# Kernel optimization log

Hardware: AMD Instinct MI355X
Metric: run time of the kernel (lower is better)

## Reference

```python
import jax, jax.numpy as jnp
import numpy as np

N = 50000      # nodes
E = 800000     # edges (before self loops)
F_IN = 256     # input features
C = 64         # out_channels per head
H = 4          # heads
NC = 3         # num_class


def setup_inputs() -> dict:
    key = jax.random.key(0)
    ks = jax.random.split(key, 11)
    s = 0.1
    return {
        "x": jax.random.normal(ks[0], (N, F_IN), jnp.float32),
        "edge_index": jax.random.randint(ks[1], (2, E), 0, N, dtype=jnp.int64),
        # conv1: in=F_IN -> H*C, concat
        "W1": jax.random.normal(ks[2], (H * C, F_IN), jnp.float32) * s,
        "as1": jax.random.normal(ks[3], (H, C), jnp.float32) * s,
        "ad1": jax.random.normal(ks[4], (H, C), jnp.float32) * s,
        "b1": jnp.zeros((H * C,), jnp.float32),
        # conv2: in=H*C -> H*C, concat
        "W2": jax.random.normal(ks[5], (H * C, H * C), jnp.float32) * s,
        "as2": jax.random.normal(ks[6], (H, C), jnp.float32) * s,
        "ad2": jax.random.normal(ks[7], (H, C), jnp.float32) * s,
        "b2": jnp.zeros((H * C,), jnp.float32),
        # conv3: in=H*C -> NC, heads averaged (concat=False)
        "W3": jax.random.normal(ks[8], (H * NC, H * C), jnp.float32) * s,
        "as3": jax.random.normal(ks[9], (H, NC), jnp.float32) * s,
        "ad3": jax.random.normal(ks[10], (H, NC), jnp.float32) * s,
        "b3": jnp.zeros((NC,), jnp.float32),
    }


def _gat_conv(x, src, dst, W, a_src, a_dst, b, concat):
    # x: [N,F]; src/dst: [E'] (self loops included); W: [H*C, F]; a_*: [H,C]
    n = x.shape[0]
    h_, c_ = a_src.shape
    h = (x @ W.T).reshape(n, h_, c_)                       # [N,H,C]
    alpha_src = (h * a_src[None]).sum(-1)                  # [N,H]
    alpha_dst = (h * a_dst[None]).sum(-1)                  # [N,H]
    e = jax.nn.leaky_relu(alpha_src[src] + alpha_dst[dst], 0.2)  # [E',H]
    # segment softmax over destination-node neighborhoods
    m = jax.ops.segment_max(e, dst, num_segments=n)        # [N,H]
    ex = jnp.exp(e - m[dst])
    den = jax.ops.segment_sum(ex, dst, num_segments=n)     # [N,H]
    alpha = ex / den[dst]                                  # [E',H]
    out = jax.ops.segment_sum(h[src] * alpha[:, :, None], dst, num_segments=n)  # [N,H,C]
    if concat:
        return out.reshape(n, h_ * c_) + b
    return out.mean(axis=1) + b


def reference(x, edge_index, W1, as1, ad1, b1, W2, as2, ad2, b2, W3, as3, ad3, b3):
    n = x.shape[0]
    loop = jnp.arange(n, dtype=edge_index.dtype)
    src = jnp.concatenate([edge_index[0], loop])  # add_self_loops=True
    dst = jnp.concatenate([edge_index[1], loop])
    x = jax.nn.elu(_gat_conv(x, src, dst, W1, as1, ad1, b1, True))
    x = jax.nn.elu(_gat_conv(x, src, dst, W2, as2, ad2, b2, True))
    x = jax.nn.elu(_gat_conv(x, src, dst, W3, as3, ad3, b3, False))
    return x
```

## Files before the change

kernel.cpp:

```cpp
#include <hip/hip_runtime.h>
#include <hip/hip_fp16.h>
#include <cstdint>
#include <cstddef>

#define NNODES 50000
#define NEDGES 800000
#define E2 (NEDGES + NNODES)
#define HC 256

typedef __attribute__((ext_vector_type(8))) short short8v;
typedef __attribute__((ext_vector_type(4))) float f32x4;
typedef const __attribute__((address_space(1))) void* gas_t;
typedef __attribute__((address_space(3))) void* las_t;


__global__ void zero_int(int* __restrict__ p, int n) {
    int i = blockIdx.x * 256 + threadIdx.x;
    if (i < n) p[i] = 0;
}

__global__ void count_deg(const int* __restrict__ ei, int* __restrict__ deg) {
    int i = blockIdx.x * 256 + threadIdx.x;
    if (i >= E2) return;
    int d = (i < NEDGES) ? ei[NEDGES + i] : (i - NEDGES);
    atomicAdd(&deg[d], 1);
}

__global__ void scan1(const int* __restrict__ deg, int* __restrict__ rp, int* __restrict__ bs) {
    __shared__ int s[256];
    int t = threadIdx.x, i = blockIdx.x * 256 + t;
    int v = (i < NNODES) ? deg[i] : 0;
    s[t] = v;
    __syncthreads();
    for (int o = 1; o < 256; o <<= 1) {
        int add = (t >= o) ? s[t - o] : 0;
        __syncthreads();
        s[t] += add;
        __syncthreads();
    }
    if (i < NNODES) rp[i] = s[t] - v;
    if (t == 255) bs[blockIdx.x] = s[255];
}

__global__ void scan2(int* __restrict__ bs, int nb) {
    __shared__ int s[256];
    int t = threadIdx.x;
    int v = (t < nb) ? bs[t] : 0;
    s[t] = v;
    __syncthreads();
    for (int o = 1; o < 256; o <<= 1) {
        int add = (t >= o) ? s[t - o] : 0;
        __syncthreads();
        s[t] += add;
        __syncthreads();
    }
    bs[t] = s[t] - v;
}

__global__ void scan3(int* __restrict__ rp, const int* __restrict__ bs, int* __restrict__ cnt) {
    int i = blockIdx.x * 256 + threadIdx.x;
    if (i < NNODES) {
        int v = rp[i] + bs[blockIdx.x];
        rp[i] = v;
        cnt[i] = v;
    }
    if (i == 0) rp[NNODES] = E2;
}

__global__ void fill_csr(const int* __restrict__ ei, int* __restrict__ cnt, int* __restrict__ csr) {
    int i = blockIdx.x * 256 + threadIdx.x;
    if (i >= E2) return;
    int s, d;
    if (i < NEDGES) { s = ei[i]; d = ei[NEDGES + i]; }
    else            { s = d = i - NEDGES; }
    int pos = atomicAdd(&cnt[d], 1);
    csr[pos] = s;
}


__device__ __forceinline__ unsigned short f2bf(float f) {
    uint32_t u = __float_as_uint(f);
    uint32_t r = (u + 0x7FFFu + ((u >> 16) & 1u)) >> 16;
    return (unsigned short)r;
}
__device__ __forceinline__ float bf2f(unsigned short h) {
    return __uint_as_float(((uint32_t)h) << 16);
}

__global__ void split_bf16(const float* __restrict__ in, unsigned short* __restrict__ hi,
                           unsigned short* __restrict__ lo, int n4) {
    int i = blockIdx.x * 256 + threadIdx.x;
    if (i >= n4) return;
    float4 v = ((const float4*)in)[i];
    unsigned short h0 = f2bf(v.x), h1 = f2bf(v.y), h2 = f2bf(v.z), h3 = f2bf(v.w);
    unsigned short l0 = f2bf(v.x - bf2f(h0));
    unsigned short l1 = f2bf(v.y - bf2f(h1));
    unsigned short l2 = f2bf(v.z - bf2f(h2));
    unsigned short l3 = f2bf(v.w - bf2f(h3));
    uint2 hp, lp;
    hp.x = (uint32_t)h0 | ((uint32_t)h1 << 16);
    hp.y = (uint32_t)h2 | ((uint32_t)h3 << 16);
    lp.x = (uint32_t)l0 | ((uint32_t)l1 << 16);
    lp.y = (uint32_t)l2 | ((uint32_t)l3 << 16);
    *(uint2*)(hi + 4 * (size_t)i) = hp;
    *(uint2*)(lo + 4 * (size_t)i) = lp;
}


__global__ __launch_bounds__(256, 2) void gemm_mfma(
    const unsigned short* __restrict__ Ah, const unsigned short* __restrict__ Al,
    const unsigned short* __restrict__ Wh, const unsigned short* __restrict__ Wl,
    _Float16* __restrict__ out16, int M) {
    __shared__ unsigned short sAh[2][128][32], sAl[2][128][32], sWh[2][128][32], sWl[2][128][32];
    const int t = threadIdx.x;
    const int m0 = blockIdx.x * 128, n0 = blockIdx.y * 128;
    const int lane = t & 63, w = t >> 6;
    const int wr = w >> 1, wc = w & 1;
    const int fr = lane & 15, fg = lane >> 4;

    const int u0 = (w * 2) * 64 + lane, u1 = (w * 2 + 1) * 64 + lane;
    const int row0 = u0 >> 2, cb0 = (u0 & 3) * 8;
    const int row1 = u1 >> 2, cb1 = (u1 & 3) * 8;
    int gra0 = m0 + row0; gra0 = gra0 < M ? gra0 : M - 1;
    int gra1 = m0 + row1; gra1 = gra1 < M ? gra1 : M - 1;
    const int grw0 = n0 + row0, grw1 = n0 + row1;

    auto stage = [&](int b, int kc) {
        __builtin_amdgcn_global_load_lds((gas_t)(Ah + (size_t)gra0 * HC + kc + cb0), (las_t)&sAh[b][row0][cb0], 16, 0, 0);
        __builtin_amdgcn_global_load_lds((gas_t)(Ah + (size_t)gra1 * HC + kc + cb1), (las_t)&sAh[b][row1][cb1], 16, 0, 0);
        __builtin_amdgcn_global_load_lds((gas_t)(Al + (size_t)gra0 * HC + kc + cb0), (las_t)&sAl[b][row0][cb0], 16, 0, 0);
        __builtin_amdgcn_global_load_lds((gas_t)(Al + (size_t)gra1 * HC + kc + cb1), (las_t)&sAl[b][row1][cb1], 16, 0, 0);
        __builtin_amdgcn_global_load_lds((gas_t)(Wh + (size_t)grw0 * HC + kc + cb0), (las_t)&sWh[b][row0][cb0], 16, 0, 0);
        __builtin_amdgcn_global_load_lds((gas_t)(Wh + (size_t)grw1 * HC + kc + cb1), (las_t)&sWh[b][row1][cb1], 16, 0, 0);
        __builtin_amdgcn_global_load_lds((gas_t)(Wl + (size_t)grw0 * HC + kc + cb0), (las_t)&sWl[b][row0][cb0], 16, 0, 0);
        __builtin_amdgcn_global_load_lds((gas_t)(Wl + (size_t)grw1 * HC + kc + cb1), (las_t)&sWl[b][row1][cb1], 16, 0, 0);
    };

    f32x4 acc[4][4];
#pragma unroll
    for (int mi = 0; mi < 4; mi++)
#pragma unroll
        for (int ni = 0; ni < 4; ni++) acc[mi][ni] = (f32x4){0.f, 0.f, 0.f, 0.f};

    auto compute = [&](int b) {
        short8v ah[4], al[4], bh[4], bl[4];
#pragma unroll
        for (int i = 0; i < 4; i++) {
            ah[i] = *(const short8v*)&sAh[b][wr * 64 + i * 16 + fr][fg * 8];
            al[i] = *(const short8v*)&sAl[b][wr * 64 + i * 16 + fr][fg * 8];
            bh[i] = *(const short8v*)&sWh[b][wc * 64 + i * 16 + fr][fg * 8];
            bl[i] = *(const short8v*)&sWl[b][wc * 64 + i * 16 + fr][fg * 8];
        }
#pragma unroll
        for (int mi = 0; mi < 4; mi++)
#pragma unroll
            for (int ni = 0; ni < 4; ni++) {
                acc[mi][ni] = __builtin_amdgcn_mfma_f32_16x16x32_bf16(ah[mi], bh[ni], acc[mi][ni], 0, 0, 0);
                acc[mi][ni] = __builtin_amdgcn_mfma_f32_16x16x32_bf16(ah[mi], bl[ni], acc[mi][ni], 0, 0, 0);
                acc[mi][ni] = __builtin_amdgcn_mfma_f32_16x16x32_bf16(al[mi], bh[ni], acc[mi][ni], 0, 0, 0);
            }
    };

    stage(0, 0);
    __syncthreads();
#pragma unroll
    for (int kt = 0; kt < 7; kt++) {
        stage((kt + 1) & 1, (kt + 1) * 32);
        compute(kt & 1);
        __syncthreads();
    }
    compute(1);

#pragma unroll
    for (int mi = 0; mi < 4; mi++) {
#pragma unroll
        for (int r = 0; r < 4; r++) {
            int gr = m0 + wr * 64 + mi * 16 + fg * 4 + r;
            if (gr < M) {
#pragma unroll
                for (int ni = 0; ni < 4; ni++) {
                    out16[(size_t)gr * HC + n0 + wc * 64 + ni * 16 + fr] = (_Float16)acc[mi][ni][r];
                }
            }
        }
    }
}


__global__ void alpha_hc(const _Float16* __restrict__ h16, const float* __restrict__ a_s,
                         const float* __restrict__ a_d, float* __restrict__ asrc,
                         float* __restrict__ adst) {
    int n = blockIdx.x * 4 + (threadIdx.x >> 6);
    int lane = threadIdx.x & 63;
    uint2 raw = *(const uint2*)(h16 + (size_t)n * HC + lane * 4);
    __half2 p0 = *(__half2*)&raw.x;
    __half2 p1 = *(__half2*)&raw.y;
    float h0 = __low2float(p0), h1 = __high2float(p0);
    float h2 = __low2float(p1), h3 = __high2float(p1);
    float4 s4 = *(const float4*)(a_s + lane * 4);
    float4 d4 = *(const float4*)(a_d + lane * 4);
    float ps = h0 * s4.x + h1 * s4.y + h2 * s4.z + h3 * s4.w;
    float pd = h0 * d4.x + h1 * d4.y + h2 * d4.z + h3 * d4.w;
#pragma unroll
    for (int o = 1; o < 16; o <<= 1) {
        ps += __shfl_xor(ps, o);
        pd += __shfl_xor(pd, o);
    }
    if ((lane & 15) == 0) {
        int hh = lane >> 4;
        asrc[n * 4 + hh] = ps;
        adst[n * 4 + hh] = pd;
    }
}


#define CHUNK 512

__global__ void aggregate_hc(const _Float16* __restrict__ h16, const float* __restrict__ asrc,
                             const float* __restrict__ adst, const int* __restrict__ rp,
                             const int* __restrict__ csr, const float* __restrict__ bias,
                             float* __restrict__ y, unsigned short* __restrict__ yh,
                             unsigned short* __restrict__ yl, int flags) {
    __shared__ int   sIdx[CHUNK];
    __shared__ float sE4[CHUNK][4];
    __shared__ float sM[4][4], sS[4][4];
    __shared__ float sRed[4][32][9];
    int n = blockIdx.x;
    int t = threadIdx.x;
    int r0 = rp[n], deg = rp[n + 1] - r0;

    if (deg <= CHUNK) {
        for (int j = t; j < deg; j += 256) sIdx[j] = csr[r0 + j];
        __syncthreads();

        int hA = t & 3, jj = t >> 2;
        float adh = adst[n * 4 + hA];
        float pm = -1e30f;
        for (int j = jj; j < deg; j += 64) {
            int s = sIdx[j];
            float e = asrc[s * 4 + hA] + adh;
            e = e > 0.f ? e : 0.2f * e;
            sE4[j][hA] = e;
            pm = fmaxf(pm, e);
        }
#pragma unroll
        for (int o = 4; o <= 32; o <<= 1) pm = fmaxf(pm, __shfl_xor(pm, o));
        if ((t & 63) < 4) sM[t >> 6][t & 3] = pm;
        __syncthreads();

        float mh = fmaxf(fmaxf(sM[0][hA], sM[1][hA]), fmaxf(sM[2][hA], sM[3][hA]));
        float ps = 0.f;
        for (int j = jj; j < deg; j += 64) {
            float ex = __expf(sE4[j][hA] - mh);
            sE4[j][hA] = ex;
            ps += ex;
        }
#pragma unroll
        for (int o = 4; o <= 32; o <<= 1) ps += __shfl_xor(ps, o);
        if ((t & 63) < 4) sS[t >> 6][t & 3] = ps;
        __syncthreads();

        int G = t >> 5, q = t & 31, hh = q >> 3;
        float a[8];
#pragma unroll
        for (int i = 0; i < 8; i++) a[i] = 0.f;
#pragma unroll 2
        for (int j = G; j < deg; j += 8) {
            int s = sIdx[j];
            float aw = sE4[j][hh];
            uint4 raw = *(const uint4*)(h16 + (size_t)s * HC + 8 * q);
            const _Float16* hv = reinterpret_cast<const _Float16*>(&raw);
#pragma unroll
            for (int i = 0; i < 8; i++) a[i] = fmaf((float)hv[i], aw, a[i]);
        }
#pragma unroll
        for (int i = 0; i < 8; i++) a[i] += __shfl_xor(a[i], 32);
        int wv = t >> 6, l = t & 63;
        if (l < 32) {
#pragma unroll
            for (int i = 0; i < 8; i++) sRed[wv][l][i] = a[i];
        }
        __syncthreads();

        int c = t;
        float val = sRed[0][c >> 3][c & 7] + sRed[1][c >> 3][c & 7]
                  + sRed[2][c >> 3][c & 7] + sRed[3][c >> 3][c & 7];
        int ch = c >> 6;
        float ssum = sS[0][ch] + sS[1][ch] + sS[2][ch] + sS[3][ch];
        float outv = val / ssum + bias[c];
        outv = outv > 0.f ? outv : expm1f(outv);
        size_t off = (size_t)n * HC + c;
        if (flags & 1) y[off] = outv;
        if (flags & 2) {
            unsigned short hi = f2bf(outv);
            yh[off] = hi;
            yl[off] = f2bf(outv - bf2f(hi));
        }
    } else {
        int w = t >> 6, l = t & 63;
        float ad = adst[n * 4 + w];
        int hoff = (w << 6) + l;
        const _Float16* hp = h16 + hoff;
        float m = -1e30f;
        for (int j = l; j < deg; j += 64) {
            int s = csr[r0 + j];
            float e = asrc[s * 4 + w] + ad;
            e = e > 0.f ? e : 0.2f * e;
            m = fmaxf(m, e);
        }
#pragma unroll
        for (int o = 32; o > 0; o >>= 1) m = fmaxf(m, __shfl_xor(m, o));
        float acc = 0.f, ssum = 0.f;
        for (int j = 0; j < deg; j++) {
            int s = csr[r0 + j];
            float e = asrc[s * 4 + w] + ad;
            e = e > 0.f ? e : 0.2f * e;
            float aa = __expf(e - m);
            ssum += aa;
            acc = fmaf(aa, (float)hp[(size_t)s * HC], acc);
        }
        float outv = acc / ssum + bias[hoff];
        outv = outv > 0.f ? outv : expm1f(outv);
        size_t off = (size_t)n * HC + hoff;
        if (flags & 1) y[off] = outv;
        if (flags & 2) {
            unsigned short hi = f2bf(outv);
            yh[off] = hi;
            yl[off] = f2bf(outv - bf2f(hi));
        }
    }
}


__global__ void gemm_small(const float* __restrict__ Y, const float* __restrict__ W3,
                           float* __restrict__ h3) {
    int idx = blockIdx.x * 256 + threadIdx.x;
    if (idx >= NNODES * 12) return;
    int n = idx / 12, o = idx - n * 12;
    const float4* xr = (const float4*)(Y + (size_t)n * HC);
    const float4* wr = (const float4*)(W3 + o * HC);
    float acc = 0.f;
#pragma unroll 8
    for (int k = 0; k < 64; k++) {
        float4 a = xr[k], b = wr[k];
        acc += a.x * b.x + a.y * b.y + a.z * b.z + a.w * b.w;
    }
    h3[idx] = acc;
}

__global__ void alpha3(const float* __restrict__ h3, const float* __restrict__ a_s,
                       const float* __restrict__ a_d, float* __restrict__ asrc,
                       float* __restrict__ adst) {
    int n = blockIdx.x * 256 + threadIdx.x;
    if (n >= NNODES) return;
    const float* hr = h3 + (size_t)n * 12;
    float s[4], d[4];
#pragma unroll
    for (int hh = 0; hh < 4; hh++) {
        s[hh] = hr[hh * 3] * a_s[hh * 3] + hr[hh * 3 + 1] * a_s[hh * 3 + 1] + hr[hh * 3 + 2] * a_s[hh * 3 + 2];
        d[hh] = hr[hh * 3] * a_d[hh * 3] + hr[hh * 3 + 1] * a_d[hh * 3 + 1] + hr[hh * 3 + 2] * a_d[hh * 3 + 2];
    }
    *(float4*)(asrc + n * 4) = make_float4(s[0], s[1], s[2], s[3]);
    *(float4*)(adst + n * 4) = make_float4(d[0], d[1], d[2], d[3]);
}

__global__ void aggregate3(const float* __restrict__ h3, const float* __restrict__ asrc,
                           const float* __restrict__ adst, const int* __restrict__ rp,
                           const int* __restrict__ csr, const float* __restrict__ b3,
                           float* __restrict__ out) {
    int n = blockIdx.x * 4 + (threadIdx.x >> 6);
    int l = threadIdx.x & 63;
    if (n >= NNODES) return;
    int r0 = rp[n], deg = rp[n + 1] - r0;
    float4 ad = *(const float4*)(adst + n * 4);

    float m0 = -1e30f, m1 = -1e30f, m2 = -1e30f, m3 = -1e30f;
    for (int j = l; j < deg; j += 64) {
        int s = csr[r0 + j];
        float4 a4 = *(const float4*)(asrc + s * 4);
        float e0 = a4.x + ad.x, e1 = a4.y + ad.y, e2 = a4.z + ad.z, e3 = a4.w + ad.w;
        e0 = e0 > 0.f ? e0 : 0.2f * e0;
        e1 = e1 > 0.f ? e1 : 0.2f * e1;
        e2 = e2 > 0.f ? e2 : 0.2f * e2;
        e3 = e3 > 0.f ? e3 : 0.2f * e3;
        m0 = fmaxf(m0, e0); m1 = fmaxf(m1, e1); m2 = fmaxf(m2, e2); m3 = fmaxf(m3, e3);
    }
    for (int o = 32; o > 0; o >>= 1) {
        m0 = fmaxf(m0, __shfl_xor(m0, o));
        m1 = fmaxf(m1, __shfl_xor(m1, o));
        m2 = fmaxf(m2, __shfl_xor(m2, o));
        m3 = fmaxf(m3, __shfl_xor(m3, o));
    }

    float acc[12];
#pragma unroll
    for (int k = 0; k < 12; k++) acc[k] = 0.f;
    float s0 = 0.f, s1 = 0.f, s2 = 0.f, s3 = 0.f;
    for (int j = l; j < deg; j += 64) {
        int s = csr[r0 + j];
        float4 a4 = *(const float4*)(asrc + s * 4);
        float e0 = a4.x + ad.x, e1 = a4.y + ad.y, e2 = a4.z + ad.z, e3 = a4.w + ad.w;
        e0 = e0 > 0.f ? e0 : 0.2f * e0;
        e1 = e1 > 0.f ? e1 : 0.2f * e1;
        e2 = e2 > 0.f ? e2 : 0.2f * e2;
        e3 = e3 > 0.f ? e3 : 0.2f * e3;
        float w0 = __expf(e0 - m0), w1 = __expf(e1 - m1), w2 = __expf(e2 - m2), w3 = __expf(e3 - m3);
        s0 += w0; s1 += w1; s2 += w2; s3 += w3;
        const float* hr = h3 + (size_t)s * 12;
#pragma unroll
        for (int c = 0; c < 3; c++) {
            acc[c]     += w0 * hr[c];
            acc[3 + c] += w1 * hr[3 + c];
            acc[6 + c] += w2 * hr[6 + c];
            acc[9 + c] += w3 * hr[9 + c];
        }
    }
    for (int o = 32; o > 0; o >>= 1) {
#pragma unroll
        for (int k = 0; k < 12; k++) acc[k] += __shfl_xor(acc[k], o);
        s0 += __shfl_xor(s0, o);
        s1 += __shfl_xor(s1, o);
        s2 += __shfl_xor(s2, o);
        s3 += __shfl_xor(s3, o);
    }
    if (l < 3) {
        float v = 0.25f * (acc[l] / s0 + acc[3 + l] / s1 + acc[6 + l] / s2 + acc[9 + l] / s3) + b3[l];
        v = v > 0.f ? v : expm1f(v);
        out[(size_t)n * 3 + l] = v;
    }
}


extern "C" void kernel_launch(void* const* d_in, const int* in_sizes, int n_in,
                              void* d_out, int out_size, void* d_ws, size_t ws_size,
                              hipStream_t stream) {
    (void)in_sizes; (void)n_in; (void)out_size; (void)ws_size;
    const float* x   = (const float*)d_in[0];
    const int*   ei  = (const int*)d_in[1];
    const float* W1  = (const float*)d_in[2];
    const float* as1 = (const float*)d_in[3];
    const float* ad1 = (const float*)d_in[4];
    const float* b1  = (const float*)d_in[5];
    const float* W2  = (const float*)d_in[6];
    const float* as2 = (const float*)d_in[7];
    const float* ad2 = (const float*)d_in[8];
    const float* b2  = (const float*)d_in[9];
    const float* W3  = (const float*)d_in[10];
    const float* as3 = (const float*)d_in[11];
    const float* ad3 = (const float*)d_in[12];
    const float* b3  = (const float*)d_in[13];
    float* out = (float*)d_out;

    uint8_t* p = (uint8_t*)d_ws;
    auto alloc = [&](size_t bytes) -> void* {
        void* r = (void*)p;
        p += (bytes + 255) & ~(size_t)255;
        return r;
    };
    float* bufY = (float*)alloc((size_t)NNODES * HC * 4);
    float* h3   = (float*)alloc((size_t)NNODES * 12 * 4);
    float* asrc = (float*)alloc((size_t)NNODES * 4 * 4);
    float* adst = (float*)alloc((size_t)NNODES * 4 * 4);
    int* deg    = (int*)alloc((size_t)NNODES * 4);
    int* rp     = (int*)alloc((size_t)(NNODES + 1) * 4);
    int* cnt    = (int*)alloc((size_t)NNODES * 4);
    int* csr    = (int*)alloc((size_t)E2 * 4);
    int* bsums  = (int*)alloc(256 * 4);
    unsigned short* xh  = (unsigned short*)alloc((size_t)NNODES * HC * 2);
    unsigned short* xl  = (unsigned short*)alloc((size_t)NNODES * HC * 2);
    unsigned short* w1h = (unsigned short*)alloc((size_t)HC * HC * 2);
    unsigned short* w1l = (unsigned short*)alloc((size_t)HC * HC * 2);
    unsigned short* w2h = (unsigned short*)alloc((size_t)HC * HC * 2);
    unsigned short* w2l = (unsigned short*)alloc((size_t)HC * HC * 2);
    _Float16* h16 = (_Float16*)alloc((size_t)NNODES * HC * 2);

    const int NB_N = (NNODES + 255) / 256;
    const int NB_E = (E2 + 255) / 256;
    const int N4_A = NNODES * HC / 4;
    const int N4_W = HC * HC / 4;

    zero_int<<<NB_N, 256, 0, stream>>>(deg, NNODES);
    count_deg<<<NB_E, 256, 0, stream>>>(ei, deg);
    scan1<<<NB_N, 256, 0, stream>>>(deg, rp, bsums);
    scan2<<<1, 256, 0, stream>>>(bsums, NB_N);
    scan3<<<NB_N, 256, 0, stream>>>(rp, bsums, cnt);
    fill_csr<<<NB_E, 256, 0, stream>>>(ei, cnt, csr);

    dim3 ggrid((NNODES + 127) / 128, 2);

    split_bf16<<<(N4_W + 255) / 256, 256, 0, stream>>>(W1, w1h, w1l, N4_W);
    split_bf16<<<(N4_A + 255) / 256, 256, 0, stream>>>(x, xh, xl, N4_A);
    gemm_mfma<<<ggrid, 256, 0, stream>>>(xh, xl, w1h, w1l, h16, NNODES);
    alpha_hc<<<NNODES / 4, 256, 0, stream>>>(h16, as1, ad1, asrc, adst);
    aggregate_hc<<<NNODES, 256, 0, stream>>>(h16, asrc, adst, rp, csr, b1, bufY, xh, xl, 2);

    split_bf16<<<(N4_W + 255) / 256, 256, 0, stream>>>(W2, w2h, w2l, N4_W);
    gemm_mfma<<<ggrid, 256, 0, stream>>>(xh, xl, w2h, w2l, h16, NNODES);
    alpha_hc<<<NNODES / 4, 256, 0, stream>>>(h16, as2, ad2, asrc, adst);
    aggregate_hc<<<NNODES, 256, 0, stream>>>(h16, asrc, adst, rp, csr, b2, bufY, xh, xl, 1);

    gemm_small<<<(NNODES * 12 + 255) / 256, 256, 0, stream>>>(bufY, W3, h3);
    alpha3<<<NB_N, 256, 0, stream>>>(h3, as3, ad3, asrc, adst);
    aggregate3<<<(NNODES + 3) / 4, 256, 0, stream>>>(h3, asrc, adst, rp, csr, b3, out);
}
```

Measured before the change: 640.2 us.

## Process eight nodes per block in GAT aggregation, one 32-thread group per node

Changes aggregate_hc from one block per destination node to eight nodes per block, each handled by a 32-thread group that does its own softmax and feature accumulation. This removes the cross-wave shared-memory reduction and cuts per-block launch and sync overhead for the many low-degree nodes. Each group now walks its edges serially with no split across wavefronts, so latency hiding per node is lower. Blocks whose total degree exceeds the smaller chunk size fall back to a serial per-node slow path, which could be costly if that happens often.

```diff
diff --git a/kernel.cpp b/kernel.cpp
--- a/kernel.cpp
+++ b/kernel.cpp
@@ -214,7 +214,8 @@
 }
 
 
-#define CHUNK 512
+#define CHUNK 384
+#define NPB 8
 
 __global__ void aggregate_hc(const _Float16* __restrict__ h16, const float* __restrict__ asrc,
                              const float* __restrict__ adst, const int* __restrict__ rp,
@@ -222,111 +223,112 @@
                              float* __restrict__ y, unsigned short* __restrict__ yh,
                              unsigned short* __restrict__ yl, int flags) {
     __shared__ int   sIdx[CHUNK];
+    __shared__ int   sOff[NPB + 1];
     __shared__ float sE4[CHUNK][4];
-    __shared__ float sM[4][4], sS[4][4];
-    __shared__ float sRed[4][32][9];
-    int n = blockIdx.x;
+    __shared__ float sM[NPB][4], sS[NPB][4];
+    __shared__ float sAd[NPB][4];
+    int n0 = blockIdx.x * NPB;
     int t = threadIdx.x;
-    int r0 = rp[n], deg = rp[n + 1] - r0;
-
-    if (deg <= CHUNK) {
-        for (int j = t; j < deg; j += 256) sIdx[j] = csr[r0 + j];
-        __syncthreads();
-
-        int hA = t & 3, jj = t >> 2;
-        float adh = adst[n * 4 + hA];
+    int r0 = rp[n0];
+    int tot = rp[n0 + NPB] - r0;
+
+    if (tot <= CHUNK) {
+        if (t <= NPB) sOff[t] = rp[n0 + t] - r0;
+        if (t >= 32 && t < 32 + NPB * 4) {
+            int i = (t - 32) >> 2, hh = t & 3;
+            sAd[i][hh] = adst[(n0 + i) * 4 + hh];
+        }
+        for (int j = t; j < tot; j += 256) sIdx[j] = csr[r0 + j];
+        __syncthreads();
+
+        int i = t >> 5, q = t & 31, hh = q >> 3, slot = q & 7;
+        int js = sOff[i], je = sOff[i + 1];
+
+        float adh = sAd[i][hh];
         float pm = -1e30f;
-        for (int j = jj; j < deg; j += 64) {
+        for (int j = js + slot; j < je; j += 8) {
             int s = sIdx[j];
-            float e = asrc[s * 4 + hA] + adh;
+            float e = asrc[s * 4 + hh] + adh;
             e = e > 0.f ? e : 0.2f * e;
-            sE4[j][hA] = e;
+            sE4[j][hh] = e;
             pm = fmaxf(pm, e);
         }
 #pragma unroll
-        for (int o = 4; o <= 32; o <<= 1) pm = fmaxf(pm, __shfl_xor(pm, o));
-        if ((t & 63) < 4) sM[t >> 6][t & 3] = pm;
-        __syncthreads();
-
-        float mh = fmaxf(fmaxf(sM[0][hA], sM[1][hA]), fmaxf(sM[2][hA], sM[3][hA]));
+        for (int o = 1; o < 8; o <<= 1) pm = fmaxf(pm, __shfl_xor(pm, o));
+        if (slot == 0) sM[i][hh] = pm;
+        __syncthreads();
+
+        float mh = sM[i][hh];
         float ps = 0.f;
-        for (int j = jj; j < deg; j += 64) {
-            float ex = __expf(sE4[j][hA] - mh);
-            sE4[j][hA] = ex;
+        for (int j = js + slot; j < je; j += 8) {
+            float ex = __expf(sE4[j][hh] - mh);
+            sE4[j][hh] = ex;
             ps += ex;
         }
 #pragma unroll
-        for (int o = 4; o <= 32; o <<= 1) ps += __shfl_xor(ps, o);
-        if ((t & 63) < 4) sS[t >> 6][t & 3] = ps;
-        __syncthreads();
-
-        int G = t >> 5, q = t & 31, hh = q >> 3;
+        for (int o = 1; o < 8; o <<= 1) ps += __shfl_xor(ps, o);
+        if (slot == 0) sS[i][hh] = ps;
+        __syncthreads();
+
         float a[8];
 #pragma unroll
-        for (int i = 0; i < 8; i++) a[i] = 0.f;
-#pragma unroll 2
-        for (int j = G; j < deg; j += 8) {
+        for (int k = 0; k < 8; k++) a[k] = 0.f;
+        for (int j = js; j < je; j++) {
             int s = sIdx[j];
             float aw = sE4[j][hh];
             uint4 raw = *(const uint4*)(h16 + (size_t)s * HC + 8 * q);
             const _Float16* hv = reinterpret_cast<const _Float16*>(&raw);
 #pragma unroll
-            for (int i = 0; i < 8; i++) a[i] = fmaf((float)hv[i], aw, a[i]);
-        }
-#pragma unroll
-        for (int i = 0; i < 8; i++) a[i] += __shfl_xor(a[i], 32);
-        int wv = t >> 6, l = t & 63;
-        if (l < 32) {
-#pragma unroll
-            for (int i = 0; i < 8; i++) sRed[wv][l][i] = a[i];
-        }
-        __syncthreads();
-
-        int c = t;
-        float val = sRed[0][c >> 3][c & 7] + sRed[1][c >> 3][c & 7]
-                  + sRed[2][c >> 3][c & 7] + sRed[3][c >> 3][c & 7];
-        int ch = c >> 6;
-        float ssum = sS[0][ch] + sS[1][ch] + sS[2][ch] + sS[3][ch];
-        float outv = val / ssum + bias[c];
-        outv = outv > 0.f ? outv : expm1f(outv);
-        size_t off = (size_t)n * HC + c;
-        if (flags & 1) y[off] = outv;
-        if (flags & 2) {
-            unsigned short hi = f2bf(outv);
-            yh[off] = hi;
-            yl[off] = f2bf(outv - bf2f(hi));
+            for (int k = 0; k < 8; k++) a[k] = fmaf((float)hv[k], aw, a[k]);
+        }
+        float inv = 1.f / sS[i][hh];
+        size_t base = (size_t)(n0 + i) * HC + 8 * q;
+#pragma unroll
+        for (int k = 0; k < 8; k++) {
+            float outv = a[k] * inv + bias[8 * q + k];
+            outv = outv > 0.f ? outv : expm1f(outv);
+            if (flags & 1) y[base + k] = outv;
+            if (flags & 2) {
+                unsigned short hi = f2bf(outv);
+                yh[base + k] = hi;
+                yl[base + k] = f2bf(outv - bf2f(hi));
+            }
         }
     } else {
-        int w = t >> 6, l = t & 63;
-        float ad = adst[n * 4 + w];
-        int hoff = (w << 6) + l;
-        const _Float16* hp = h16 + hoff;
-        float m = -1e30f;
-        for (int j = l; j < deg; j += 64) {
-            int s = csr[r0 + j];
-            float e = asrc[s * 4 + w] + ad;
-            e = e > 0.f ? e : 0.2f * e;
-            m = fmaxf(m, e);
-        }
-#pragma unroll
-        for (int o = 32; o > 0; o >>= 1) m = fmaxf(m, __shfl_xor(m, o));
-        float acc = 0.f, ssum = 0.f;
-        for (int j = 0; j < deg; j++) {
-            int s = csr[r0 + j];
-            float e = asrc[s * 4 + w] + ad;
-            e = e > 0.f ? e : 0.2f * e;
-            float aa = __expf(e - m);
-            ssum += aa;
-            acc = fmaf(aa, (float)hp[(size_t)s * HC], acc);
-        }
-        float outv = acc / ssum + bias[hoff];
-        outv = outv > 0.f ? outv : expm1f(outv);
-        size_t off = (size_t)n * HC + hoff;
-        if (flags & 1) y[off] = outv;
-        if (flags & 2) {
-            unsigned short hi = f2bf(outv);
-            yh[off] = hi;
-            yl[off] = f2bf(outv - bf2f(hi));
+        for (int i = 0; i < NPB; i++) {
+            int n = n0 + i;
+            int rr0 = rp[n], deg = rp[n + 1] - rr0;
+            int w = t >> 6, l = t & 63;
+            float ad = adst[n * 4 + w];
+            int hoff = (w << 6) + l;
+            const _Float16* hp = h16 + hoff;
+            float m = -1e30f;
+            for (int j = l; j < deg; j += 64) {
+                int s = csr[rr0 + j];
+                float e = asrc[s * 4 + w] + ad;
+                e = e > 0.f ? e : 0.2f * e;
+                m = fmaxf(m, e);
+            }
+#pragma unroll
+            for (int o = 32; o > 0; o >>= 1) m = fmaxf(m, __shfl_xor(m, o));
+            float acc = 0.f, ssum = 0.f;
+            for (int j = 0; j < deg; j++) {
+                int s = csr[rr0 + j];
+                float e = asrc[s * 4 + w] + ad;
+                e = e > 0.f ? e : 0.2f * e;
+                float aa = __expf(e - m);
+                ssum += aa;
+                acc = fmaf(aa, (float)hp[(size_t)s * HC], acc);
+            }
+            float outv = acc / ssum + bias[hoff];
+            outv = outv > 0.f ? outv : expm1f(outv);
+            size_t off = (size_t)n * HC + hoff;
+            if (flags & 1) y[off] = outv;
+            if (flags & 2) {
+                unsigned short hi = f2bf(outv);
+                yh[off] = hi;
+                yl[off] = f2bf(outv - bf2f(hi));
+            }
         }
     }
 }
@@ -492,12 +494,12 @@
     split_bf16<<<(N4_A + 255) / 256, 256, 0, stream>>>(x, xh, xl, N4_A);
     gemm_mfma<<<ggrid, 256, 0, stream>>>(xh, xl, w1h, w1l, h16, NNODES);
     alpha_hc<<<NNODES / 4, 256, 0, stream>>>(h16, as1, ad1, asrc, adst);
-    aggregate_hc<<<NNODES, 256, 0, stream>>>(h16, asrc, adst, rp, csr, b1, bufY, xh, xl, 2);
+    aggregate_hc<<<NNODES / NPB, 256, 0, stream>>>(h16, asrc, adst, rp, csr, b1, bufY, xh, xl, 2);
 
     split_bf16<<<(N4_W + 255) / 256, 256, 0, stream>>>(W2, w2h, w2l, N4_W);
     gemm_mfma<<<ggrid, 256, 0, stream>>>(xh, xl, w2h, w2l, h16, NNODES);
     alpha_hc<<<NNODES / 4, 256, 0, stream>>>(h16, as2, ad2, asrc, adst);
-    aggregate_hc<<<NNODES, 256, 0, stream>>>(h16, asrc, adst, rp, csr, b2, bufY, xh, xl, 1);
+    aggregate_hc<<<NNODES / NPB, 256, 0, stream>>>(h16, asrc, adst, rp, csr, b2, bufY, xh, xl, 1);
 
     gemm_small<<<(NNODES * 12 + 255) / 256, 256, 0, stream>>>(bufY, W3, h3);
     alpha3<<<NB_N, 256, 0, stream>>>(h3, as3, ad3, asrc, adst);
```

New measurement: 640.0 us. Within noise of the previous version (-0.0%).
